# Performance work log

Hardware: AMD Instinct MI355X
Metric: run time of the kernel (lower is better)

## Reference

```python
import jax, jax.numpy as jnp
import numpy as np

LAMBDA_SCALE = 0.5
EPS = 1e-6

def setup_inputs() -> dict:
    key = jax.random.key(0)
    ks = jax.random.split(key, 9)
    B, S, D, E, F = 4, 2048, 1024, 8, 4096
    x = jax.random.normal(ks[0], (B, S, D), dtype=jnp.float32)
    prev_logits = jax.random.normal(ks[1], (B, S, E), dtype=jnp.float32)
    # router params (nn.Linear default init scale ~ 1/sqrt(fan_in))
    Wt = jax.random.normal(ks[2], (E, D), dtype=jnp.float32) / np.sqrt(D)
    Wgt = jax.random.normal(ks[3], (E, E), dtype=jnp.float32) / np.sqrt(E)
    We_logits = jnp.zeros((E,), dtype=jnp.float32)
    # expert MLPs, stacked over the expert axis
    W1 = jax.random.normal(ks[4], (E, D, F), dtype=jnp.float32) / np.sqrt(D)
    b1 = jax.random.normal(ks[5], (E, F), dtype=jnp.float32) * 0.01
    W2 = jax.random.normal(ks[6], (E, F, D), dtype=jnp.float32) / np.sqrt(F)
    b2 = jax.random.normal(ks[7], (E, D), dtype=jnp.float32) * 0.01
    return {"x": x, "prev_logits": prev_logits, "Wt": Wt, "Wgt": Wgt,
            "We_logits": We_logits, "W1": W1, "b1": b1, "W2": W2, "b2": b2}

def reference(x, prev_logits, Wt, Wgt, We_logits, W1, b1, W2, b2):
    # router logits: [B,S,E]
    logits = jnp.einsum('bsd,ed->bse', x, Wt) + jnp.einsum('bse,fe->bsf', prev_logits, Wgt)
    st = jax.nn.softmax(logits, axis=-1)
    We = jax.nn.sigmoid(We_logits)                      # [E]
    mask = (st > LAMBDA_SCALE * We).astype(st.dtype)    # data-dependent gate mask
    g = st * mask                                       # [B,S,E]
    # dense per-expert MLP over all tokens (faithful to the module)
    h = jax.nn.gelu(jnp.einsum('bsd,edf->bsef', x, W1) + b1, approximate=False)  # [B,S,E,F]
    outk = jnp.einsum('bsef,efd->bsed', h, W2) + b2     # [B,S,E,D]
    y = jnp.einsum('bse,bsed->bsd', g, outk)
    y = y / (jnp.sum(g, axis=-1, keepdims=True) + EPS)
    return (y, jax.lax.stop_gradient(logits))
```

## Files before the change

kernel.cpp:

```cpp
#include <hip/hip_runtime.h>
#include <math.h>

#define NTOK 8192
#define DDIM 1024
#define NEXP 8
#define FDIM 4096
#define MAXROWS 26624

typedef short bf16x8 __attribute__((ext_vector_type(8)));
typedef float f32x4 __attribute__((ext_vector_type(4)));

#define BAR() asm volatile("s_barrier" ::: "memory")
#define WAITV(n) asm volatile("s_waitcnt vmcnt(" #n ")" ::: "memory")

static __device__ __forceinline__ unsigned short f2bf(float f) {
  unsigned int u = __float_as_uint(f);
  u += 0x7fffu + ((u >> 16) & 1u);
  return (unsigned short)(u >> 16);
}
static __device__ __forceinline__ float bf2f(unsigned short b) {
  return __uint_as_float(((unsigned int)b) << 16);
}

static __device__ __forceinline__ void gl_lds16(const void* g, void* l) {
  __builtin_amdgcn_global_load_lds(
      (const __attribute__((address_space(1))) unsigned int*)g,
      (__attribute__((address_space(3))) unsigned int*)l, 16, 0, 0);
}

static __device__ __forceinline__ float gelu_f(float v) {
  float x2 = v * v;
  float p = fmaf(x2, 0.10294422f, 2.3021183f);
  float E = __builtin_amdgcn_exp2f(v * p);
  return v - v * __builtin_amdgcn_rcpf(E + 1.f);
}

__global__ __launch_bounds__(256) void router_kernel(
    const float* __restrict__ x, const float* __restrict__ prev,
    const float* __restrict__ Wt, const float* __restrict__ Wgt,
    const float* __restrict__ Wel,
    float* __restrict__ gn, float* __restrict__ logits_out)
{
  __shared__ float wt_s[NEXP * DDIM];
  const int tid = threadIdx.x;
  for (int i = tid; i < NEXP * DDIM; i += 256) wt_s[i] = Wt[i];
  __syncthreads();
  const int lane = tid & 63;
  const int t = blockIdx.x * 4 + (tid >> 6);

  const float* xr = x + (size_t)t * DDIM;
  float acc[NEXP];
#pragma unroll
  for (int e = 0; e < NEXP; ++e) acc[e] = 0.f;
  for (int k = lane; k < DDIM; k += 64) {
    float xv = xr[k];
#pragma unroll
    for (int e = 0; e < NEXP; ++e) acc[e] += xv * wt_s[e * DDIM + k];
  }
#pragma unroll
  for (int e = 0; e < NEXP; ++e) {
    float v = acc[e];
#pragma unroll
    for (int off = 32; off >= 1; off >>= 1) v += __shfl_xor(v, off);
    acc[e] = v;
  }
  float pl[NEXP];
#pragma unroll
  for (int e = 0; e < NEXP; ++e) pl[e] = prev[(size_t)t * NEXP + e];
#pragma unroll
  for (int e = 0; e < NEXP; ++e) {
    float s = acc[e];
#pragma unroll
    for (int e2 = 0; e2 < NEXP; ++e2) s += pl[e2] * Wgt[e * NEXP + e2];
    acc[e] = s;
  }
  float mx = acc[0];
#pragma unroll
  for (int e = 1; e < NEXP; ++e) mx = fmaxf(mx, acc[e]);
  float st[NEXP]; float se = 0.f;
#pragma unroll
  for (int e = 0; e < NEXP; ++e) { st[e] = expf(acc[e] - mx); se += st[e]; }
  float inv = 1.f / se;
  float g[NEXP]; float gs = 0.f;
#pragma unroll
  for (int e = 0; e < NEXP; ++e) {
    float s = st[e] * inv;
    float we = 1.f / (1.f + expf(-Wel[e]));
    float gg = (s > 0.5f * we) ? s : 0.f;
    g[e] = gg; gs += gg;
  }
  float r = 1.f / (gs + 1e-6f);
  if (lane < NEXP) {
    gn[(size_t)t * NEXP + lane] = g[lane] * r;
    logits_out[(size_t)t * NEXP + lane] = acc[lane];
  }
}

__global__ __launch_bounds__(256) void cast_kernel(
    const float* __restrict__ in, unsigned short* __restrict__ out)
{
  size_t i = ((size_t)blockIdx.x * 256 + threadIdx.x) * 8;
  float4 a = *(const float4*)(in + i);
  float4 b = *(const float4*)(in + i + 4);
  unsigned short tb[8];
  tb[0]=f2bf(a.x); tb[1]=f2bf(a.y); tb[2]=f2bf(a.z); tb[3]=f2bf(a.w);
  tb[4]=f2bf(b.x); tb[5]=f2bf(b.y); tb[6]=f2bf(b.z); tb[7]=f2bf(b.w);
  *(uint4*)(out + i) = *(const uint4*)tb;
}

__global__ __launch_bounds__(256) void count_kernel(
    const float* __restrict__ gn, int* __restrict__ cnt)
{
  const int e = blockIdx.x, tid = threadIdx.x;
  int c = 0;
  for (int t = tid; t < NTOK; t += 256) c += (gn[(size_t)t * NEXP + e] > 0.f) ? 1 : 0;
#pragma unroll
  for (int o = 32; o >= 1; o >>= 1) c += __shfl_xor(c, o);
  __shared__ int sm[4];
  if ((tid & 63) == 0) sm[tid >> 6] = c;
  __syncthreads();
  if (tid == 0) cnt[e] = sm[0] + sm[1] + sm[2] + sm[3];
}

__global__ __launch_bounds__(256) void compact_kernel(
    const float* __restrict__ gn, const int* __restrict__ cnt,
    int* __restrict__ offs, int* __restrict__ rowtok, int* __restrict__ rowof)
{
  const int e = blockIdx.x, tid = threadIdx.x;
  int base = 0;
#pragma unroll
  for (int q = 0; q < 8; ++q) if (q < e) base += (cnt[q] + 255) & ~255;
  const int padcnt = (cnt[e] + 255) & ~255;
  if (e == 0 && tid == 0) {
    int a = 0; offs[0] = 0;
#pragma unroll
    for (int q = 0; q < 8; ++q) { a += (cnt[q] + 255) & ~255; offs[q + 1] = a; }
  }
  __shared__ int wsm[4];
  __shared__ int running;
  if (tid == 0) running = 0;
  __syncthreads();
  const int lane = tid & 63, wv = tid >> 6;
  for (int c0 = 0; c0 < NTOK; c0 += 256) {
    const int t = c0 + tid;
    const bool pr = gn[(size_t)t * NEXP + e] > 0.f;
    unsigned long long bal = __ballot(pr);
    int pre = __popcll(bal & ((1ull << lane) - 1ull));
    if (lane == 0) wsm[wv] = __popcll(bal);
    __syncthreads();
    int wbase = 0;
#pragma unroll
    for (int q = 0; q < 4; ++q) if (q < wv) wbase += wsm[q];
    const int tot = wsm[0] + wsm[1] + wsm[2] + wsm[3];
    const int idx = base + running + wbase + pre;
    if (pr) rowtok[idx] = t;
    rowof[(size_t)t * NEXP + e] = pr ? idx : -1;
    __syncthreads();
    if (tid == 0) running += tot;
  }
  __syncthreads();
  for (int i = cnt[e] + tid; i < padcnt; i += 256) rowtok[base + i] = -1;
}

__global__ __launch_bounds__(256) void y_init_kernel(
    const float* __restrict__ gn, const float* __restrict__ b2,
    float* __restrict__ y)
{
  const int t = blockIdx.y;
  const int d = blockIdx.x * 256 + threadIdx.x;
  float s = 0.f;
#pragma unroll
  for (int e = 0; e < NEXP; ++e) s += gn[(size_t)t * NEXP + e] * b2[(size_t)e * DDIM + d];
  y[(size_t)t * DDIM + d] = s;
}

__global__ __launch_bounds__(256) void transcvt(
    const float* __restrict__ in, unsigned short* __restrict__ out,
    int Kin, int Nin)
{
  __shared__ float tile[64][65];
  const size_t zo = (size_t)blockIdx.z * Kin * Nin;
  const float* inp = in + zo;
  unsigned short* outp = out + zo;
  const int k0 = blockIdx.y * 64, n0 = blockIdx.x * 64;
  const int tid = threadIdx.x;
  const int r = tid >> 4, c4 = (tid & 15) * 4;
#pragma unroll
  for (int rr = 0; rr < 64; rr += 16) {
    float4 v = *(const float4*)(inp + (size_t)(k0 + r + rr) * Nin + n0 + c4);
    tile[r + rr][c4] = v.x; tile[r + rr][c4 + 1] = v.y;
    tile[r + rr][c4 + 2] = v.z; tile[r + rr][c4 + 3] = v.w;
  }
  __syncthreads();
#pragma unroll
  for (int it = 0; it < 2; ++it) {
    const int o = it * 256 + tid;
    const int n = o >> 3, ks = (o & 7) * 8;
    unsigned short tb[8];
#pragma unroll
    for (int j = 0; j < 8; ++j) tb[j] = f2bf(tile[ks + j][n]);
    *(uint4*)(outp + (size_t)(n0 + n) * Kin + k0 + ks) = *(const uint4*)tb;
  }
}


__global__ __launch_bounds__(512, 2) void gemm_h256(
    const unsigned short* __restrict__ xb,
    const unsigned short* __restrict__ W,
    const float* __restrict__ b1,
    const float* __restrict__ gn,
    const int* __restrict__ rowtok,
    const int* __restrict__ offs,
    unsigned short* __restrict__ hb)
{
  __shared__ unsigned short As[2][256 * 64];
  __shared__ unsigned short Bs[2][256 * 64];
  __shared__ float gns[256];
  __shared__ float b1s[256];
  __shared__ int toks[256];
  const int tid = threadIdx.x;
  const int r0 = blockIdx.y * 256;
  if (r0 >= offs[8]) return;
  int e = 0;
#pragma unroll
  for (int q = 1; q < 8; ++q) if (r0 >= offs[q]) e = q;
  const int n0 = blockIdx.x * 256;
  const unsigned short* We = W + (size_t)e * FDIM * DDIM;

  if (tid < 256) {
    const int tk = rowtok[r0 + tid];
    toks[tid] = tk;
    gns[tid] = (tk >= 0) ? gn[(size_t)tk * NEXP + e] : 0.f;
    b1s[tid] = b1[(size_t)e * FDIM + n0 + tid];
  }
  __syncthreads();

  const int rc = tid >> 3;
  const int gld = tid & 7;
  const int gsrc = gld ^ (rc & 7);
  const unsigned short* aP[4];
  const unsigned short* bP[4];
#pragma unroll
  for (int c = 0; c < 4; ++c) {
    int tk = toks[c * 64 + rc]; if (tk < 0) tk = 0;
    aP[c] = xb + (size_t)tk * DDIM + gsrc * 8;
    bP[c] = We + (size_t)(n0 + c * 64 + rc) * DDIM + gsrc * 8;
  }

  const int lane = tid & 63;
  const int wid = tid >> 6;
  const int wm = (wid >> 2) * 128;
  const int wn = (wid & 3) * 64;
  const int fr = lane & 15;
  const int q4 = lane >> 4;

  f32x4 acc[8][4];
#pragma unroll
  for (int i = 0; i < 8; ++i)
#pragma unroll
    for (int j = 0; j < 4; ++j) acc[i][j] = (f32x4){0.f, 0.f, 0.f, 0.f};

  auto stA = [&](int kt, int b, int c) { gl_lds16(aP[c] + kt * 64, &As[b][c * 4096 + tid * 8]); };
  auto stB = [&](int kt, int b, int c) { gl_lds16(bP[c] + kt * 64, &Bs[b][c * 4096 + tid * 8]); };
  auto rdA = [&](int cur, int i, int kk) -> bf16x8 {
    const int row = wm + i * 16 + fr;
    const int sl = (kk * 4 + q4) ^ (row & 7);
    return *(const bf16x8*)&As[cur][row * 64 + sl * 8];
  };
  auto rdB = [&](int cur, int j, int kk) -> bf16x8 {
    const int row = wn + j * 16 + fr;
    const int sl = (kk * 4 + q4) ^ (row & 7);
    return *(const bf16x8*)&Bs[cur][row * 64 + sl * 8];
  };

  const int NT = DDIM / 64;
  bf16x8 aX[4][2], aY[4][2], bb[2][2];

#pragma unroll
  for (int c = 0; c < 4; ++c) { stA(0, 0, c); stB(0, 0, c); }
  WAITV(0); BAR();

  for (int t = 0; t < NT - 1; ++t) {
    const int cur = t & 1, nxt = cur ^ 1;
    stA(t + 1, nxt, 0); stA(t + 1, nxt, 1);
    WAITV(2); BAR();
#pragma unroll
    for (int i = 0; i < 4; ++i) { aX[i][0] = rdA(cur, i, 0); aX[i][1] = rdA(cur, i, 1); }
#pragma unroll
    for (int j = 0; j < 2; ++j) { bb[j][0] = rdB(cur, j, 0); bb[j][1] = rdB(cur, j, 1); }
    __builtin_amdgcn_s_setprio(1);
#pragma unroll
    for (int i = 0; i < 4; ++i)
#pragma unroll
      for (int j = 0; j < 2; ++j)
#pragma unroll
        for (int kk = 0; kk < 2; ++kk)
          acc[i][j] = __builtin_amdgcn_mfma_f32_16x16x32_bf16(aX[i][kk], bb[j][kk], acc[i][j], 0, 0, 0);
    __builtin_amdgcn_s_setprio(0);
    stA(t + 1, nxt, 2); stA(t + 1, nxt, 3);
#pragma unroll
    for (int i = 0; i < 4; ++i) { aY[i][0] = rdA(cur, 4 + i, 0); aY[i][1] = rdA(cur, 4 + i, 1); }
    __builtin_amdgcn_s_setprio(1);
#pragma unroll
    for (int i = 0; i < 4; ++i)
#pragma unroll
      for (int j = 0; j < 2; ++j)
#pragma unroll
        for (int kk = 0; kk < 2; ++kk)
          acc[4 + i][j] = __builtin_amdgcn_mfma_f32_16x16x32_bf16(aY[i][kk], bb[j][kk], acc[4 + i][j], 0, 0, 0);
    __builtin_amdgcn_s_setprio(0);
    stB(t + 1, nxt, 0); stB(t + 1, nxt, 1);
#pragma unroll
    for (int j = 0; j < 2; ++j) { bb[j][0] = rdB(cur, 2 + j, 0); bb[j][1] = rdB(cur, 2 + j, 1); }
    __builtin_amdgcn_s_setprio(1);
#pragma unroll
    for (int i = 0; i < 4; ++i)
#pragma unroll
      for (int j = 0; j < 2; ++j)
#pragma unroll
        for (int kk = 0; kk < 2; ++kk)
          acc[4 + i][2 + j] = __builtin_amdgcn_mfma_f32_16x16x32_bf16(aY[i][kk], bb[j][kk], acc[4 + i][2 + j], 0, 0, 0);
    __builtin_amdgcn_s_setprio(0);
    stB(t + 1, nxt, 2); stB(t + 1, nxt, 3);
    __builtin_amdgcn_s_setprio(1);
#pragma unroll
    for (int i = 0; i < 4; ++i)
#pragma unroll
      for (int j = 0; j < 2; ++j)
#pragma unroll
        for (int kk = 0; kk < 2; ++kk)
          acc[i][2 + j] = __builtin_amdgcn_mfma_f32_16x16x32_bf16(aX[i][kk], bb[j][kk], acc[i][2 + j], 0, 0, 0);
    __builtin_amdgcn_s_setprio(0);
    BAR();
  }
  {
    const int cur = (NT - 1) & 1;
    WAITV(0); BAR();
#pragma unroll
    for (int i = 0; i < 4; ++i) { aX[i][0] = rdA(cur, i, 0); aX[i][1] = rdA(cur, i, 1); }
#pragma unroll
    for (int i = 0; i < 4; ++i) { aY[i][0] = rdA(cur, 4 + i, 0); aY[i][1] = rdA(cur, 4 + i, 1); }
#pragma unroll
    for (int j = 0; j < 2; ++j) { bb[j][0] = rdB(cur, j, 0); bb[j][1] = rdB(cur, j, 1); }
#pragma unroll
    for (int i = 0; i < 4; ++i)
#pragma unroll
      for (int j = 0; j < 2; ++j)
#pragma unroll
        for (int kk = 0; kk < 2; ++kk) {
          acc[i][j] = __builtin_amdgcn_mfma_f32_16x16x32_bf16(aX[i][kk], bb[j][kk], acc[i][j], 0, 0, 0);
          acc[4 + i][j] = __builtin_amdgcn_mfma_f32_16x16x32_bf16(aY[i][kk], bb[j][kk], acc[4 + i][j], 0, 0, 0);
        }
#pragma unroll
    for (int j = 0; j < 2; ++j) { bb[j][0] = rdB(cur, 2 + j, 0); bb[j][1] = rdB(cur, 2 + j, 1); }
#pragma unroll
    for (int i = 0; i < 4; ++i)
#pragma unroll
      for (int j = 0; j < 2; ++j)
#pragma unroll
        for (int kk = 0; kk < 2; ++kk) {
          acc[i][2 + j] = __builtin_amdgcn_mfma_f32_16x16x32_bf16(aX[i][kk], bb[j][kk], acc[i][2 + j], 0, 0, 0);
          acc[4 + i][2 + j] = __builtin_amdgcn_mfma_f32_16x16x32_bf16(aY[i][kk], bb[j][kk], acc[4 + i][2 + j], 0, 0, 0);
        }
  }

#pragma unroll
  for (int i = 0; i < 8; ++i)
#pragma unroll
    for (int rr = 0; rr < 4; ++rr) {
      const int row = wm + i * 16 + q4 * 4 + rr;
      const int tk = toks[row];
      if (tk < 0) continue;
      const float gv = gns[row];
      unsigned short* hrow = hb + (size_t)(r0 + row) * FDIM + n0;
#pragma unroll
      for (int j = 0; j < 4; ++j) {
        const int col = wn + j * 16 + fr;
        hrow[col] = f2bf(gelu_f(acc[i][j][rr] + b1s[col]) * gv);
      }
    }
}

__global__ __launch_bounds__(512, 2) void gemm_o256(
    const unsigned short* __restrict__ hb,
    const unsigned short* __restrict__ W,
    const int* __restrict__ offs,
    unsigned short* __restrict__ hb2)
{
  __shared__ unsigned short As[2][256 * 64];
  __shared__ unsigned short Bs[2][256 * 64];
  const int tid = threadIdx.x;
  const int r0 = blockIdx.y * 256;
  if (r0 >= offs[8]) return;
  int e = 0;
#pragma unroll
  for (int q = 1; q < 8; ++q) if (r0 >= offs[q]) e = q;
  const int n0 = blockIdx.x * 256;
  const unsigned short* We = W + (size_t)e * FDIM * DDIM;

  const int rc = tid >> 3;
  const int gld = tid & 7;
  const int gsrc = gld ^ (rc & 7);
  const unsigned short* aP[4];
  const unsigned short* bP[4];
#pragma unroll
  for (int c = 0; c < 4; ++c) {
    aP[c] = hb + (size_t)(r0 + c * 64 + rc) * FDIM + gsrc * 8;
    bP[c] = We + (size_t)(n0 + c * 64 + rc) * FDIM + gsrc * 8;
  }

  const int lane = tid & 63;
  const int wid = tid >> 6;
  const int wm = (wid >> 2) * 128;
  const int wn = (wid & 3) * 64;
  const int fr = lane & 15;
  const int q4 = lane >> 4;

  f32x4 acc[8][4];
#pragma unroll
  for (int i = 0; i < 8; ++i)
#pragma unroll
    for (int j = 0; j < 4; ++j) acc[i][j] = (f32x4){0.f, 0.f, 0.f, 0.f};

  auto stA = [&](int kt, int b, int c) { gl_lds16(aP[c] + kt * 64, &As[b][c * 4096 + tid * 8]); };
  auto stB = [&](int kt, int b, int c) { gl_lds16(bP[c] + kt * 64, &Bs[b][c * 4096 + tid * 8]); };
  auto rdA = [&](int cur, int i, int kk) -> bf16x8 {
    const int row = wm + i * 16 + fr;
    const int sl = (kk * 4 + q4) ^ (row & 7);
    return *(const bf16x8*)&As[cur][row * 64 + sl * 8];
  };
  auto rdB = [&](int cur, int j, int kk) -> bf16x8 {
    const int row = wn + j * 16 + fr;
    const int sl = (kk * 4 + q4) ^ (row & 7);
    return *(const bf16x8*)&Bs[cur][row * 64 + sl * 8];
  };

  const int NT = FDIM / 64;
  bf16x8 aX[4][2], aY[4][2], bb[2][2];

#pragma unroll
  for (int c = 0; c < 4; ++c) { stA(0, 0, c); stB(0, 0, c); }
  WAITV(0); BAR();

  for (int t = 0; t < NT - 1; ++t) {
    const int cur = t & 1, nxt = cur ^ 1;
    stA(t + 1, nxt, 0); stA(t + 1, nxt, 1);
    WAITV(2); BAR();
#pragma unroll
    for (int i = 0; i < 4; ++i) { aX[i][0] = rdA(cur, i, 0); aX[i][1] = rdA(cur, i, 1); }
#pragma unroll
    for (int j = 0; j < 2; ++j) { bb[j][0] = rdB(cur, j, 0); bb[j][1] = rdB(cur, j, 1); }
    __builtin_amdgcn_s_setprio(1);
#pragma unroll
    for (int i = 0; i < 4; ++i)
#pragma unroll
      for (int j = 0; j < 2; ++j)
#pragma unroll
        for (int kk = 0; kk < 2; ++kk)
          acc[i][j] = __builtin_amdgcn_mfma_f32_16x16x32_bf16(aX[i][kk], bb[j][kk], acc[i][j], 0, 0, 0);
    __builtin_amdgcn_s_setprio(0);
    stA(t + 1, nxt, 2); stA(t + 1, nxt, 3);
#pragma unroll
    for (int i = 0; i < 4; ++i) { aY[i][0] = rdA(cur, 4 + i, 0); aY[i][1] = rdA(cur, 4 + i, 1); }
    __builtin_amdgcn_s_setprio(1);
#pragma unroll
    for (int i = 0; i < 4; ++i)
#pragma unroll
      for (int j = 0; j < 2; ++j)
#pragma unroll
        for (int kk = 0; kk < 2; ++kk)
          acc[4 + i][j] = __builtin_amdgcn_mfma_f32_16x16x32_bf16(aY[i][kk], bb[j][kk], acc[4 + i][j], 0, 0, 0);
    __builtin_amdgcn_s_setprio(0);
    stB(t + 1, nxt, 0); stB(t + 1, nxt, 1);
#pragma unroll
    for (int j = 0; j < 2; ++j) { bb[j][0] = rdB(cur, 2 + j, 0); bb[j][1] = rdB(cur, 2 + j, 1); }
    __builtin_amdgcn_s_setprio(1);
#pragma unroll
    for (int i = 0; i < 4; ++i)
#pragma unroll
      for (int j = 0; j < 2; ++j)
#pragma unroll
        for (int kk = 0; kk < 2; ++kk)
          acc[4 + i][2 + j] = __builtin_amdgcn_mfma_f32_16x16x32_bf16(aY[i][kk], bb[j][kk], acc[4 + i][2 + j], 0, 0, 0);
    __builtin_amdgcn_s_setprio(0);
    stB(t + 1, nxt, 2); stB(t + 1, nxt, 3);
    __builtin_amdgcn_s_setprio(1);
#pragma unroll
    for (int i = 0; i < 4; ++i)
#pragma unroll
      for (int j = 0; j < 2; ++j)
#pragma unroll
        for (int kk = 0; kk < 2; ++kk)
          acc[i][2 + j] = __builtin_amdgcn_mfma_f32_16x16x32_bf16(aX[i][kk], bb[j][kk], acc[i][2 + j], 0, 0, 0);
    __builtin_amdgcn_s_setprio(0);
    BAR();
  }
  {
    const int cur = (NT - 1) & 1;
    WAITV(0); BAR();
#pragma unroll
    for (int i = 0; i < 4; ++i) { aX[i][0] = rdA(cur, i, 0); aX[i][1] = rdA(cur, i, 1); }
#pragma unroll
    for (int i = 0; i < 4; ++i) { aY[i][0] = rdA(cur, 4 + i, 0); aY[i][1] = rdA(cur, 4 + i, 1); }
#pragma unroll
    for (int j = 0; j < 2; ++j) { bb[j][0] = rdB(cur, j, 0); bb[j][1] = rdB(cur, j, 1); }
#pragma unroll
    for (int i = 0; i < 4; ++i)
#pragma unroll
      for (int j = 0; j < 2; ++j)
#pragma unroll
        for (int kk = 0; kk < 2; ++kk) {
          acc[i][j] = __builtin_amdgcn_mfma_f32_16x16x32_bf16(aX[i][kk], bb[j][kk], acc[i][j], 0, 0, 0);
          acc[4 + i][j] = __builtin_amdgcn_mfma_f32_16x16x32_bf16(aY[i][kk], bb[j][kk], acc[4 + i][j], 0, 0, 0);
        }
#pragma unroll
    for (int j = 0; j < 2; ++j) { bb[j][0] = rdB(cur, 2 + j, 0); bb[j][1] = rdB(cur, 2 + j, 1); }
#pragma unroll
    for (int i = 0; i < 4; ++i)
#pragma unroll
      for (int j = 0; j < 2; ++j)
#pragma unroll
        for (int kk = 0; kk < 2; ++kk) {
          acc[i][2 + j] = __builtin_amdgcn_mfma_f32_16x16x32_bf16(aX[i][kk], bb[j][kk], acc[i][2 + j], 0, 0, 0);
          acc[4 + i][2 + j] = __builtin_amdgcn_mfma_f32_16x16x32_bf16(aY[i][kk], bb[j][kk], acc[4 + i][2 + j], 0, 0, 0);
        }
  }

#pragma unroll
  for (int i = 0; i < 8; ++i)
#pragma unroll
    for (int rr = 0; rr < 4; ++rr) {
      const int row = wm + i * 16 + q4 * 4 + rr;
      unsigned short* orow = hb2 + (size_t)(r0 + row) * DDIM + n0;
#pragma unroll
      for (int j = 0; j < 4; ++j) {
        const int col = wn + j * 16 + fr;
        orow[col] = f2bf(acc[i][j][rr]);
      }
    }
}

__global__ __launch_bounds__(256) void combine_kernel(
    const unsigned short* __restrict__ hb2, const int* __restrict__ rowof,
    const float* __restrict__ gn, const float* __restrict__ b2,
    float* __restrict__ y)
{
  const int t = blockIdx.y;
  const int d = blockIdx.x * 256 + threadIdx.x;
  float s = 0.f;
#pragma unroll
  for (int e = 0; e < NEXP; ++e) {
    s += gn[(size_t)t * NEXP + e] * b2[(size_t)e * DDIM + d];
    const int r = rowof[(size_t)t * NEXP + e];
    if (r >= 0) s += bf2f(hb2[(size_t)r * DDIM + d]);
  }
  y[(size_t)t * DDIM + d] = s;
}

__global__ __launch_bounds__(128, 2) void gemm_h128(
    const unsigned short* __restrict__ xb,
    const unsigned short* __restrict__ W,
    const float* __restrict__ b1,
    const float* __restrict__ gn,
    const int* __restrict__ rowtok,
    const int* __restrict__ offs,
    int efix,
    unsigned short* __restrict__ hb)
{
  __shared__ unsigned short As[2][4096];
  __shared__ unsigned short Bs[2][4096];
  __shared__ float gns[128];
  __shared__ float b1s[128];
  __shared__ int toks[128];
  const int tid = threadIdx.x;
  const int e = efix;
  const int hbase = offs[e];
  const int mt = (hbase >> 7) + blockIdx.y;
  if (mt * 128 >= offs[e + 1]) return;
  const int n0 = blockIdx.x * 128;
  const unsigned short* We = W;

  {
    const int tk = rowtok[mt * 128 + tid];
    toks[tid] = tk;
    gns[tid] = (tk >= 0) ? gn[(size_t)tk * NEXP + e] : 0.f;
    b1s[tid] = b1[(size_t)e * FDIM + n0 + tid];
  }
  __syncthreads();

  const int st_row = tid >> 2;
  const int st_off = (((tid & 3) ^ (st_row & 3)) << 3);
  const unsigned short* aP[4];
  const unsigned short* bP[4];
#pragma unroll
  for (int i = 0; i < 4; ++i) {
    int tk = toks[i * 32 + st_row]; if (tk < 0) tk = 0;
    aP[i] = xb + (size_t)tk * DDIM + st_off;
    bP[i] = We + (size_t)(n0 + i * 32 + st_row) * DDIM + st_off;
  }
  const int ldst = tid * 8;
  const int lane = tid & 63;
  const int w = tid >> 6;
  const int fr = lane & 15;
  const int rdoff = (((lane >> 4) ^ (lane & 3)) << 3);

  f32x4 acc[8][4];
#pragma unroll
  for (int i = 0; i < 8; ++i)
#pragma unroll
    for (int j = 0; j < 4; ++j) acc[i][j] = (f32x4){0.f, 0.f, 0.f, 0.f};

  auto stage = [&](int kt, int b) {
    const int ke = kt * 32;
#pragma unroll
    for (int i = 0; i < 4; ++i) {
      gl_lds16(aP[i] + ke, &As[b][i * 1024 + ldst]);
      gl_lds16(bP[i] + ke, &Bs[b][i * 1024 + ldst]);
    }
  };

  const int NT = DDIM / 32;
  stage(0, 0);
  asm volatile("s_waitcnt vmcnt(0) lgkmcnt(0)" ::: "memory"); BAR();
  for (int t = 0; t < NT; ++t) {
    const int cur = t & 1;
    if (t + 1 < NT) stage(t + 1, cur ^ 1);
    bf16x8 af[8], bfv[4];
#pragma unroll
    for (int i = 0; i < 8; ++i) af[i] = *(const bf16x8*)&As[cur][(i * 16 + fr) * 32 + rdoff];
#pragma unroll
    for (int j = 0; j < 4; ++j) bfv[j] = *(const bf16x8*)&Bs[cur][(w * 64 + j * 16 + fr) * 32 + rdoff];
#pragma unroll
    for (int i = 0; i < 8; ++i)
#pragma unroll
      for (int j = 0; j < 4; ++j)
        acc[i][j] = __builtin_amdgcn_mfma_f32_16x16x32_bf16(af[i], bfv[j], acc[i][j], 0, 0, 0);
    if (t + 1 < NT) { asm volatile("s_waitcnt vmcnt(0) lgkmcnt(0)" ::: "memory"); BAR(); }
  }
#pragma unroll
  for (int i = 0; i < 8; ++i)
#pragma unroll
    for (int r = 0; r < 4; ++r) {
      const int row = i * 16 + (lane >> 4) * 4 + r;
      const int tk = toks[row];
      if (tk < 0) continue;
      const float gv = gns[row];
      unsigned short* hrow = hb + (size_t)(mt * 128 + row - hbase) * FDIM + n0;
#pragma unroll
      for (int j = 0; j < 4; ++j) {
        const int col = w * 64 + j * 16 + fr;
        hrow[col] = f2bf(gelu_f(acc[i][j][r] + b1s[col]) * gv);
      }
    }
}

__global__ __launch_bounds__(128, 2) void gemm_o128(
    const unsigned short* __restrict__ hb,
    const unsigned short* __restrict__ W,
    const int* __restrict__ rowtok,
    const int* __restrict__ offs,
    int efix,
    float* __restrict__ yout)
{
  __shared__ unsigned short As[2][4096];
  __shared__ unsigned short Bs[2][4096];
  __shared__ int toks[128];
  const int tid = threadIdx.x;
  const int e = efix;
  const int hbase = offs[e];
  const int mt = (hbase >> 7) + blockIdx.y;
  if (mt * 128 >= offs[e + 1]) return;
  const int n0 = blockIdx.x * 128;

  toks[tid] = rowtok[mt * 128 + tid];
  __syncthreads();

  const int st_row = tid >> 2;
  const int st_off = (((tid & 3) ^ (st_row & 3)) << 3);
  const unsigned short* aP[4];
  const unsigned short* bP[4];
#pragma unroll
  for (int i = 0; i < 4; ++i) {
    aP[i] = hb + (size_t)(mt * 128 - hbase + i * 32 + st_row) * FDIM + st_off;
    bP[i] = W + (size_t)(n0 + i * 32 + st_row) * FDIM + st_off;
  }
  const int ldst = tid * 8;
  const int lane = tid & 63;
  const int w = tid >> 6;
  const int fr = lane & 15;
  const int rdoff = (((lane >> 4) ^ (lane & 3)) << 3);

  f32x4 acc[8][4];
#pragma unroll
  for (int i = 0; i < 8; ++i)
#pragma unroll
    for (int j = 0; j < 4; ++j) acc[i][j] = (f32x4){0.f, 0.f, 0.f, 0.f};

  auto stage = [&](int kt, int b) {
    const int ke = kt * 32;
#pragma unroll
    for (int i = 0; i < 4; ++i) {
      gl_lds16(aP[i] + ke, &As[b][i * 1024 + ldst]);
      gl_lds16(bP[i] + ke, &Bs[b][i * 1024 + ldst]);
    }
  };

  const int NT = FDIM / 32;
  stage(0, 0);
  asm volatile("s_waitcnt vmcnt(0) lgkmcnt(0)" ::: "memory"); BAR();
  for (int t = 0; t < NT; ++t) {
    const int cur = t & 1;
    if (t + 1 < NT) stage(t + 1, cur ^ 1);
    bf16x8 af[8], bfv[4];
#pragma unroll
    for (int i = 0; i < 8; ++i) af[i] = *(const bf16x8*)&As[cur][(i * 16 + fr) * 32 + rdoff];
#pragma unroll
    for (int j = 0; j < 4; ++j) bfv[j] = *(const bf16x8*)&Bs[cur][(w * 64 + j * 16 + fr) * 32 + rdoff];
#pragma unroll
    for (int i = 0; i < 8; ++i)
#pragma unroll
      for (int j = 0; j < 4; ++j)
        acc[i][j] = __builtin_amdgcn_mfma_f32_16x16x32_bf16(af[i], bfv[j], acc[i][j], 0, 0, 0);
    if (t + 1 < NT) { asm volatile("s_waitcnt vmcnt(0) lgkmcnt(0)" ::: "memory"); BAR(); }
  }
#pragma unroll
  for (int i = 0; i < 8; ++i)
#pragma unroll
    for (int r = 0; r < 4; ++r) {
      const int row = i * 16 + (lane >> 4) * 4 + r;
      const int tk = toks[row];
      if (tk < 0) continue;
      float* yrow = yout + (size_t)tk * DDIM + n0;
#pragma unroll
      for (int j = 0; j < 4; ++j) {
        const int col = w * 64 + j * 16 + fr;
        yrow[col] += acc[i][j][r];
      }
    }
}

extern "C" void kernel_launch(void* const* d_in, const int* in_sizes, int n_in,
                              void* d_out, int out_size, void* d_ws, size_t ws_size,
                              hipStream_t stream) {
  (void)in_sizes; (void)n_in; (void)out_size;
  const float* x    = (const float*)d_in[0];
  const float* prev = (const float*)d_in[1];
  const float* Wt   = (const float*)d_in[2];
  const float* Wgt  = (const float*)d_in[3];
  const float* Wel  = (const float*)d_in[4];
  const float* W1   = (const float*)d_in[5];
  const float* b1   = (const float*)d_in[6];
  const float* W2   = (const float*)d_in[7];
  const float* b2   = (const float*)d_in[8];

  float* y      = (float*)d_out;
  float* logits = y + (size_t)NTOK * DDIM;

  char* ws = (char*)d_ws;
  size_t pos = 0;
  auto take = [&](size_t bytes) -> char* {
    char* r = ws + pos; pos += (bytes + 255) & ~(size_t)255; return r;
  };
  float* gn            = (float*)take((size_t)NTOK * NEXP * 4);
  int* cnt             = (int*)take(64);
  int* offs            = (int*)take(64);
  int* rowtok          = (int*)take((size_t)MAXROWS * 4);
  int* rowof           = (int*)take((size_t)NTOK * NEXP * 4);
  unsigned short* xb   = (unsigned short*)take((size_t)NTOK * DDIM * 2);
  const size_t fixed = pos;

  const size_t wexp = (size_t)FDIM * DDIM;
  const size_t needA = fixed + 2 * NEXP * wexp * 2 + (size_t)MAXROWS * FDIM * 2
                       + (size_t)MAXROWS * DDIM * 2 + 4096;
  const bool tierA = ws_size >= needA;

  router_kernel<<<dim3(NTOK / 4), dim3(256), 0, stream>>>(x, prev, Wt, Wgt, Wel, gn, logits);
  cast_kernel<<<dim3((NTOK * DDIM) / (8 * 256)), dim3(256), 0, stream>>>(x, xb);
  count_kernel<<<dim3(NEXP), dim3(256), 0, stream>>>(gn, cnt);
  compact_kernel<<<dim3(NEXP), dim3(256), 0, stream>>>(gn, cnt, offs, rowtok, rowof);

  if (tierA) {
    unsigned short* W1b = (unsigned short*)take(NEXP * wexp * 2);
    unsigned short* W2b = (unsigned short*)take(NEXP * wexp * 2);
    unsigned short* hb  = (unsigned short*)take((size_t)MAXROWS * FDIM * 2);
    unsigned short* hb2 = (unsigned short*)take((size_t)MAXROWS * DDIM * 2);

    transcvt<<<dim3(FDIM / 64, DDIM / 64, NEXP), dim3(256), 0, stream>>>(W1, W1b, DDIM, FDIM);
    transcvt<<<dim3(DDIM / 64, FDIM / 64, NEXP), dim3(256), 0, stream>>>(W2, W2b, FDIM, DDIM);
    gemm_h256<<<dim3(FDIM / 256, MAXROWS / 256), dim3(512), 0, stream>>>(
        xb, W1b, b1, gn, rowtok, offs, hb);
    gemm_o256<<<dim3(DDIM / 256, MAXROWS / 256), dim3(512), 0, stream>>>(
        hb, W2b, offs, hb2);
    combine_kernel<<<dim3(DDIM / 256, NTOK), dim3(256), 0, stream>>>(hb2, rowof, gn, b2, y);
  } else {
    unsigned short* Wb = (unsigned short*)take(wexp * 2);
    unsigned short* hb = (unsigned short*)take((size_t)NTOK * FDIM * 2);

    y_init_kernel<<<dim3(DDIM / 256, NTOK), dim3(256), 0, stream>>>(gn, b2, y);
    for (int e = 0; e < NEXP; ++e) {
      transcvt<<<dim3(FDIM / 64, DDIM / 64, 1), dim3(256), 0, stream>>>(
          W1 + (size_t)e * wexp, Wb, DDIM, FDIM);
      gemm_h128<<<dim3(FDIM / 128, 64), dim3(128), 0, stream>>>(
          xb, Wb, b1, gn, rowtok, offs, e, hb);
      transcvt<<<dim3(DDIM / 64, FDIM / 64, 1), dim3(256), 0, stream>>>(
          W2 + (size_t)e * wexp, Wb, FDIM, DDIM);
      gemm_o128<<<dim3(DDIM / 128, 64), dim3(128), 0, stream>>>(
          hb, Wb, rowtok, offs, e, y);
    }
  }
}
```

Baseline: 500.9 us.

## Issue full next-tile prefetch up front and swizzle workgroups across XCDs

Both grouped expert GEMM kernels now issue all global-to-LDS loads for the next K tile at the top of each iteration, right after a full vmcnt(0) wait and barrier. Previously those loads were interleaved between MFMA groups, and the separate epilogue iteration is gone. A sched_barrier keeps the compiler from moving these loads. The kernels also remap workgroup IDs so that consecutive blocks share an XCD, aiming for better L2 reuse of weight and activation tiles. The trade-off is a loss of fine-grained overlap: the full wait each iteration could stall if loads are not done by the next tile, and the trailing barrier was removed, which relies on the leading barrier to protect the double buffer.

```diff
diff --git a/kernel.cpp b/kernel.cpp
--- a/kernel.cpp
+++ b/kernel.cpp
@@ -11,7 +11,7 @@
 typedef float f32x4 __attribute__((ext_vector_type(4)));
 
 #define BAR() asm volatile("s_barrier" ::: "memory")
-#define WAITV(n) asm volatile("s_waitcnt vmcnt(" #n ")" ::: "memory")
+#define WAITV0() asm volatile("s_waitcnt vmcnt(0)" ::: "memory")
 
 static __device__ __forceinline__ unsigned short f2bf(float f) {
   unsigned int u = __float_as_uint(f);
@@ -33,6 +33,14 @@
   float p = fmaf(x2, 0.10294422f, 2.3021183f);
   float E = __builtin_amdgcn_exp2f(v * p);
   return v - v * __builtin_amdgcn_rcpf(E + 1.f);
+}
+
+static __device__ __forceinline__ void xcd_swz(int& bx, int& by, int gx, int gy) {
+  const int nwg = gx * gy;
+  const int lin = by * gx + bx;
+  const int cpx = nwg >> 3;
+  const int swz = (lin & 7) * cpx + (lin >> 3);
+  bx = swz % gx; by = swz / gx;
 }
 
 __global__ __launch_bounds__(256) void router_kernel(
@@ -219,12 +227,14 @@
   __shared__ float b1s[256];
   __shared__ int toks[256];
   const int tid = threadIdx.x;
-  const int r0 = blockIdx.y * 256;
+  int bx = blockIdx.x, by = blockIdx.y;
+  xcd_swz(bx, by, gridDim.x, gridDim.y);
+  const int r0 = by * 256;
   if (r0 >= offs[8]) return;
   int e = 0;
 #pragma unroll
   for (int q = 1; q < 8; ++q) if (r0 >= offs[q]) e = q;
-  const int n0 = blockIdx.x * 256;
+  const int n0 = bx * 256;
   const unsigned short* We = W + (size_t)e * FDIM * DDIM;
 
   if (tid < 256) {
@@ -260,8 +270,13 @@
 #pragma unroll
     for (int j = 0; j < 4; ++j) acc[i][j] = (f32x4){0.f, 0.f, 0.f, 0.f};
 
-  auto stA = [&](int kt, int b, int c) { gl_lds16(aP[c] + kt * 64, &As[b][c * 4096 + tid * 8]); };
-  auto stB = [&](int kt, int b, int c) { gl_lds16(bP[c] + kt * 64, &Bs[b][c * 4096 + tid * 8]); };
+  auto stAll = [&](int kt, int b) {
+#pragma unroll
+    for (int c = 0; c < 4; ++c) {
+      gl_lds16(aP[c] + kt * 64, &As[b][c * 4096 + tid * 8]);
+      gl_lds16(bP[c] + kt * 64, &Bs[b][c * 4096 + tid * 8]);
+    }
+  };
   auto rdA = [&](int cur, int i, int kk) -> bf16x8 {
     const int row = wm + i * 16 + fr;
     const int sl = (kk * 4 + q4) ^ (row & 7);
@@ -276,14 +291,12 @@
   const int NT = DDIM / 64;
   bf16x8 aX[4][2], aY[4][2], bb[2][2];
 
-#pragma unroll
-  for (int c = 0; c < 4; ++c) { stA(0, 0, c); stB(0, 0, c); }
-  WAITV(0); BAR();
-
-  for (int t = 0; t < NT - 1; ++t) {
+  stAll(0, 0);
+  for (int t = 0; t < NT; ++t) {
     const int cur = t & 1, nxt = cur ^ 1;
-    stA(t + 1, nxt, 0); stA(t + 1, nxt, 1);
-    WAITV(2); BAR();
+    WAITV0(); BAR();
+    if (t + 1 < NT) stAll(t + 1, nxt);
+    __builtin_amdgcn_sched_barrier(0);
 #pragma unroll
     for (int i = 0; i < 4; ++i) { aX[i][0] = rdA(cur, i, 0); aX[i][1] = rdA(cur, i, 1); }
 #pragma unroll
@@ -297,7 +310,6 @@
         for (int kk = 0; kk < 2; ++kk)
           acc[i][j] = __builtin_amdgcn_mfma_f32_16x16x32_bf16(aX[i][kk], bb[j][kk], acc[i][j], 0, 0, 0);
     __builtin_amdgcn_s_setprio(0);
-    stA(t + 1, nxt, 2); stA(t + 1, nxt, 3);
 #pragma unroll
     for (int i = 0; i < 4; ++i) { aY[i][0] = rdA(cur, 4 + i, 0); aY[i][1] = rdA(cur, 4 + i, 1); }
     __builtin_amdgcn_s_setprio(1);
@@ -309,7 +321,6 @@
         for (int kk = 0; kk < 2; ++kk)
           acc[4 + i][j] = __builtin_amdgcn_mfma_f32_16x16x32_bf16(aY[i][kk], bb[j][kk], acc[4 + i][j], 0, 0, 0);
     __builtin_amdgcn_s_setprio(0);
-    stB(t + 1, nxt, 0); stB(t + 1, nxt, 1);
 #pragma unroll
     for (int j = 0; j < 2; ++j) { bb[j][0] = rdB(cur, 2 + j, 0); bb[j][1] = rdB(cur, 2 + j, 1); }
     __builtin_amdgcn_s_setprio(1);
@@ -321,7 +332,6 @@
         for (int kk = 0; kk < 2; ++kk)
           acc[4 + i][2 + j] = __builtin_amdgcn_mfma_f32_16x16x32_bf16(aY[i][kk], bb[j][kk], acc[4 + i][2 + j], 0, 0, 0);
     __builtin_amdgcn_s_setprio(0);
-    stB(t + 1, nxt, 2); stB(t + 1, nxt, 3);
     __builtin_amdgcn_s_setprio(1);
 #pragma unroll
     for (int i = 0; i < 4; ++i)
@@ -331,37 +341,6 @@
         for (int kk = 0; kk < 2; ++kk)
           acc[i][2 + j] = __builtin_amdgcn_mfma_f32_16x16x32_bf16(aX[i][kk], bb[j][kk], acc[i][2 + j], 0, 0, 0);
     __builtin_amdgcn_s_setprio(0);
-    BAR();
-  }
-  {
-    const int cur = (NT - 1) & 1;
-    WAITV(0); BAR();
-#pragma unroll
-    for (int i = 0; i < 4; ++i) { aX[i][0] = rdA(cur, i, 0); aX[i][1] = rdA(cur, i, 1); }
-#pragma unroll
-    for (int i = 0; i < 4; ++i) { aY[i][0] = rdA(cur, 4 + i, 0); aY[i][1] = rdA(cur, 4 + i, 1); }
-#pragma unroll
-    for (int j = 0; j < 2; ++j) { bb[j][0] = rdB(cur, j, 0); bb[j][1] = rdB(cur, j, 1); }
-#pragma unroll
-    for (int i = 0; i < 4; ++i)
-#pragma unroll
-      for (int j = 0; j < 2; ++j)
-#pragma unroll
-        for (int kk = 0; kk < 2; ++kk) {
-          acc[i][j] = __builtin_amdgcn_mfma_f32_16x16x32_bf16(aX[i][kk], bb[j][kk], acc[i][j], 0, 0, 0);
-          acc[4 + i][j] = __builtin_amdgcn_mfma_f32_16x16x32_bf16(aY[i][kk], bb[j][kk], acc[4 + i][j], 0, 0, 0);
-        }
-#pragma unroll
-    for (int j = 0; j < 2; ++j) { bb[j][0] = rdB(cur, 2 + j, 0); bb[j][1] = rdB(cur, 2 + j, 1); }
-#pragma unroll
-    for (int i = 0; i < 4; ++i)
-#pragma unroll
-      for (int j = 0; j < 2; ++j)
-#pragma unroll
-        for (int kk = 0; kk < 2; ++kk) {
-          acc[i][2 + j] = __builtin_amdgcn_mfma_f32_16x16x32_bf16(aX[i][kk], bb[j][kk], acc[i][2 + j], 0, 0, 0);
-          acc[4 + i][2 + j] = __builtin_amdgcn_mfma_f32_16x16x32_bf16(aY[i][kk], bb[j][kk], acc[4 + i][2 + j], 0, 0, 0);
-        }
   }
 
 #pragma unroll
@@ -390,12 +369,14 @@
   __shared__ unsigned short As[2][256 * 64];
   __shared__ unsigned short Bs[2][256 * 64];
   const int tid = threadIdx.x;
-  const int r0 = blockIdx.y * 256;
+  int bx = blockIdx.x, by = blockIdx.y;
+  xcd_swz(bx, by, gridDim.x, gridDim.y);
+  const int r0 = by * 256;
   if (r0 >= offs[8]) return;
   int e = 0;
 #pragma unroll
   for (int q = 1; q < 8; ++q) if (r0 >= offs[q]) e = q;
-  const int n0 = blockIdx.x * 256;
+  const int n0 = bx * 256;
   const unsigned short* We = W + (size_t)e * FDIM * DDIM;
 
   const int rc = tid >> 3;
@@ -422,8 +403,13 @@
 #pragma unroll
     for (int j = 0; j < 4; ++j) acc[i][j] = (f32x4){0.f, 0.f, 0.f, 0.f};
 
-  auto stA = [&](int kt, int b, int c) { gl_lds16(aP[c] + kt * 64, &As[b][c * 4096 + tid * 8]); };
-  auto stB = [&](int kt, int b, int c) { gl_lds16(bP[c] + kt * 64, &Bs[b][c * 4096 + tid * 8]); };
+  auto stAll = [&](int kt, int b) {
+#pragma unroll
+    for (int c = 0; c < 4; ++c) {
+      gl_lds16(aP[c] + kt * 64, &As[b][c * 4096 + tid * 8]);
+      gl_lds16(bP[c] + kt * 64, &Bs[b][c * 4096 + tid * 8]);
+    }
+  };
   auto rdA = [&](int cur, int i, int kk) -> bf16x8 {
     const int row = wm + i * 16 + fr;
     const int sl = (kk * 4 + q4) ^ (row & 7);
@@ -438,14 +424,12 @@
   const int NT = FDIM / 64;
   bf16x8 aX[4][2], aY[4][2], bb[2][2];
 
-#pragma unroll
-  for (int c = 0; c < 4; ++c) { stA(0, 0, c); stB(0, 0, c); }
-  WAITV(0); BAR();
-
-  for (int t = 0; t < NT - 1; ++t) {
+  stAll(0, 0);
+  for (int t = 0; t < NT; ++t) {
     const int cur = t & 1, nxt = cur ^ 1;
-    stA(t + 1, nxt, 0); stA(t + 1, nxt, 1);
-    WAITV(2); BAR();
+    WAITV0(); BAR();
+    if (t + 1 < NT) stAll(t + 1, nxt);
+    __builtin_amdgcn_sched_barrier(0);
 #pragma unroll
     for (int i = 0; i < 4; ++i) { aX[i][0] = rdA(cur, i, 0); aX[i][1] = rdA(cur, i, 1); }
 #pragma unroll
@@ -459,7 +443,6 @@
         for (int kk = 0; kk < 2; ++kk)
           acc[i][j] = __builtin_amdgcn_mfma_f32_16x16x32_bf16(aX[i][kk], bb[j][kk], acc[i][j], 0, 0, 0);
     __builtin_amdgcn_s_setprio(0);
-    stA(t + 1, nxt, 2); stA(t + 1, nxt, 3);
 #pragma unroll
     for (int i = 0; i < 4; ++i) { aY[i][0] = rdA(cur, 4 + i, 0); aY[i][1] = rdA(cur, 4 + i, 1); }
     __builtin_amdgcn_s_setprio(1);
@@ -471,7 +454,6 @@
         for (int kk = 0; kk < 2; ++kk)
           acc[4 + i][j] = __builtin_amdgcn_mfma_f32_16x16x32_bf16(aY[i][kk], bb[j][kk], acc[4 + i][j], 0, 0, 0);
     __builtin_amdgcn_s_setprio(0);
-    stB(t + 1, nxt, 0); stB(t + 1, nxt, 1);
 #pragma unroll
     for (int j = 0; j < 2; ++j) { bb[j][0] = rdB(cur, 2 + j, 0); bb[j][1] = rdB(cur, 2 + j, 1); }
     __builtin_amdgcn_s_setprio(1);
@@ -483,7 +465,6 @@
         for (int kk = 0; kk < 2; ++kk)
           acc[4 + i][2 + j] = __builtin_amdgcn_mfma_f32_16x16x32_bf16(aY[i][kk], bb[j][kk], acc[4 + i][2 + j], 0, 0, 0);
     __builtin_amdgcn_s_setprio(0);
-    stB(t + 1, nxt, 2); stB(t + 1, nxt, 3);
     __builtin_amdgcn_s_setprio(1);
 #pragma unroll
     for (int i = 0; i < 4; ++i)
@@ -493,37 +474,6 @@
         for (int kk = 0; kk < 2; ++kk)
           acc[i][2 + j] = __builtin_amdgcn_mfma_f32_16x16x32_bf16(aX[i][kk], bb[j][kk], acc[i][2 + j], 0, 0, 0);
     __builtin_amdgcn_s_setprio(0);
-    BAR();
-  }
-  {
-    const int cur = (NT - 1) & 1;
-    WAITV(0); BAR();
-#pragma unroll
-    for (int i = 0; i < 4; ++i) { aX[i][0] = rdA(cur, i, 0); aX[i][1] = rdA(cur, i, 1); }
-#pragma unroll
-    for (int i = 0; i < 4; ++i) { aY[i][0] = rdA(cur, 4 + i, 0); aY[i][1] = rdA(cur, 4 + i, 1); }
-#pragma unroll
-    for (int j = 0; j < 2; ++j) { bb[j][0] = rdB(cur, j, 0); bb[j][1] = rdB(cur, j, 1); }
-#pragma unroll
-    for (int i = 0; i < 4; ++i)
-#pragma unroll
-      for (int j = 0; j < 2; ++j)
-#pragma unroll
-        for (int kk = 0; kk < 2; ++kk) {
-          acc[i][j] = __builtin_amdgcn_mfma_f32_16x16x32_bf16(aX[i][kk], bb[j][kk], acc[i][j], 0, 0, 0);
-          acc[4 + i][j] = __builtin_amdgcn_mfma_f32_16x16x32_bf16(aY[i][kk], bb[j][kk], acc[4 + i][j], 0, 0, 0);
-        }
-#pragma unroll
-    for (int j = 0; j < 2; ++j) { bb[j][0] = rdB(cur, 2 + j, 0); bb[j][1] = rdB(cur, 2 + j, 1); }
-#pragma unroll
-    for (int i = 0; i < 4; ++i)
-#pragma unroll
-      for (int j = 0; j < 2; ++j)
-#pragma unroll
-        for (int kk = 0; kk < 2; ++kk) {
-          acc[i][2 + j] = __builtin_amdgcn_mfma_f32_16x16x32_bf16(aX[i][kk], bb[j][kk], acc[i][2 + j], 0, 0, 0);
-          acc[4 + i][2 + j] = __builtin_amdgcn_mfma_f32_16x16x32_bf16(aY[i][kk], bb[j][kk], acc[4 + i][2 + j], 0, 0, 0);
-        }
   }
 
 #pragma unroll
```

New measurement: 763.7 us. 1.52x slower.
